# Optimization experiments

Measured on AMD Instinct MI355X. Metric: run time of the kernel, lower is better.

Reference implementation:

```python
import jax, jax.numpy as jnp
import numpy as np

N_NODES = 50000
N_EDGES = 800000
F_IN = 128
HEADS = 4
C_OUT = 32
HID = HEADS * C_OUT  # 128
NEG_SLOPE = 0.2


def _gatv2_layer(x, src, dst, W_l, b_l, W_r, b_r, att, bias, concat):
    """PyG-style GATv2Conv (eval mode, no dropout).
    x: [N, F]; W_*: [F, H*C]; att: [H, C]; bias: [H*C] (concat) or [C] (mean).
    """
    N = x.shape[0]
    H, C = att.shape
    x_l = (x @ W_l + b_l).reshape(N, H, C)  # source transform
    x_r = (x @ W_r + b_r).reshape(N, H, C)  # target transform
    e = jax.nn.leaky_relu(x_l[src] + x_r[dst], NEG_SLOPE)      # [E, H, C]
    logits = jnp.einsum('ehc,hc->eh', e, att)                   # [E, H]
    # segment softmax over incoming edges of each destination node
    m = jax.ops.segment_max(logits, dst, num_segments=N)        # [N, H]
    alpha = jnp.exp(logits - m[dst])
    denom = jax.ops.segment_sum(alpha, dst, num_segments=N)     # [N, H]
    alpha = alpha / (denom[dst] + 1e-16)
    out = jax.ops.segment_sum(x_l[src] * alpha[..., None], dst, num_segments=N)  # [N, H, C]
    out = out.reshape(N, H * C) if concat else out.mean(axis=1)
    return out + bias


def setup_inputs() -> dict:
    key = jax.random.key(0)
    ks = jax.random.split(key, 20)
    s = 0.1
    inp = {
        'x': jax.random.normal(ks[0], (N_NODES, F_IN), dtype=jnp.float32),
        'edge_index': jax.random.randint(ks[1], (2, N_EDGES), 0, N_NODES, dtype=jnp.int64),
        # layer 1: 128 -> 4 heads x 32
        'W_l1': jax.random.normal(ks[2], (F_IN, HID), dtype=jnp.float32) * s,
        'b_l1': jnp.zeros((HID,), dtype=jnp.float32),
        'W_r1': jax.random.normal(ks[3], (F_IN, HID), dtype=jnp.float32) * s,
        'b_r1': jnp.zeros((HID,), dtype=jnp.float32),
        'att1': jax.random.normal(ks[4], (HEADS, C_OUT), dtype=jnp.float32) * s,
        'bias1': jnp.zeros((HID,), dtype=jnp.float32),
        # layer 2: 128 -> 4 heads x 32
        'W_l2': jax.random.normal(ks[5], (HID, HID), dtype=jnp.float32) * s,
        'b_l2': jnp.zeros((HID,), dtype=jnp.float32),
        'W_r2': jax.random.normal(ks[6], (HID, HID), dtype=jnp.float32) * s,
        'b_r2': jnp.zeros((HID,), dtype=jnp.float32),
        'att2': jax.random.normal(ks[7], (HEADS, C_OUT), dtype=jnp.float32) * s,
        'bias2': jnp.zeros((HID,), dtype=jnp.float32),
        # final layer: 128 -> 1 head x 1, concat=False
        'W_l3': jax.random.normal(ks[8], (HID, 1), dtype=jnp.float32) * s,
        'b_l3': jnp.zeros((1,), dtype=jnp.float32),
        'W_r3': jax.random.normal(ks[9], (HID, 1), dtype=jnp.float32) * s,
        'b_r3': jnp.zeros((1,), dtype=jnp.float32),
        'att3': jax.random.normal(ks[10], (1, 1), dtype=jnp.float32) * s,
        'bias3': jnp.zeros((1,), dtype=jnp.float32),
    }
    return inp


def reference(x, edge_index, W_l1, b_l1, W_r1, b_r1, att1, bias1,
              W_l2, b_l2, W_r2, b_r2, att2, bias2,
              W_l3, b_l3, W_r3, b_r3, att3, bias3):
    src, dst = edge_index[0], edge_index[1]
    h = jax.nn.elu(_gatv2_layer(x, src, dst, W_l1, b_l1, W_r1, b_r1, att1, bias1, True))
    h = jax.nn.elu(_gatv2_layer(h, src, dst, W_l2, b_l2, W_r2, b_r2, att2, bias2, True))
    o = _gatv2_layer(h, src, dst, W_l3, b_l3, W_r3, b_r3, att3, bias3, False)
    return jax.nn.sigmoid(o).reshape(x.shape[0], 1)
```

## Files before the change

### kernel.cpp

```cpp
#include <hip/hip_runtime.h>
#include <hip/hip_bf16.h>
#include <math.h>

#define NN 50000
#define NE 800000
#define NBUK 391
#define BNODES 128

typedef __attribute__((ext_vector_type(8))) short bf16x8;
typedef __attribute__((ext_vector_type(4))) float f32x4;
typedef __attribute__((ext_vector_type(8))) unsigned short ushort8v;

__device__ __forceinline__ ushort f2bf(float v) {
  __hip_bfloat16 h = __float2bfloat16(v);
  return *(ushort*)&h;
}
__device__ __forceinline__ float bf2f(ushort u) {
  return __uint_as_float(((unsigned int)u) << 16);
}

__global__ void pack_w(const float* __restrict__ Wl, const float* __restrict__ Wr,
                       ushort* __restrict__ Bpack) {
  int t = blockIdx.x * 256 + threadIdx.x;
  if (t >= 4096) return;
  int hi = t & 3;
  int col = (t >> 2) & 255;
  int kt = t >> 10;
  const float* W = (col < 128) ? (Wl + col) : (Wr + (col - 128));
  ushort4 u0, u1;
  int k0 = kt * 32 + hi * 8;
  u0.x = f2bf(W[(k0 + 0) * 128]); u0.y = f2bf(W[(k0 + 1) * 128]);
  u0.z = f2bf(W[(k0 + 2) * 128]); u0.w = f2bf(W[(k0 + 3) * 128]);
  u1.x = f2bf(W[(k0 + 4) * 128]); u1.y = f2bf(W[(k0 + 5) * 128]);
  u1.z = f2bf(W[(k0 + 6) * 128]); u1.w = f2bf(W[(k0 + 7) * 128]);
  *(ushort4*)&Bpack[t * 8] = u0;
  *(ushort4*)&Bpack[t * 8 + 4] = u1;
}

template <int AF32>
__global__ __launch_bounds__(256) void gemm_mfma(
    const void* __restrict__ Aptr, const ushort* __restrict__ Bpack,
    const float* __restrict__ bl, const float* __restrict__ br,
    ushort* __restrict__ Xl, ushort* __restrict__ Xr, int n) {
  __shared__ ushort tile[64][264];
  const int tid = threadIdx.x;
  const int wv = tid >> 6;
  const int l = tid & 63;
  const int lr = l & 15;
  const int hi = l >> 4;
  const int r0 = blockIdx.x * 64;

  f32x4 acc[4][4];
#pragma unroll
  for (int mi = 0; mi < 4; ++mi)
#pragma unroll
    for (int nj = 0; nj < 4; ++nj) acc[mi][nj] = (f32x4)0.f;

#pragma unroll
  for (int kt = 0; kt < 4; ++kt) {
    bf16x8 b[4], a[4];
#pragma unroll
    for (int nj = 0; nj < 4; ++nj) {
      int col = wv * 64 + nj * 16 + lr;
      b[nj] = *(const bf16x8*)&Bpack[((kt * 256 + col) * 4 + hi) * 8];
    }
#pragma unroll
    for (int mi = 0; mi < 4; ++mi) {
      int row = r0 + mi * 16 + lr;
      row = row < n ? row : n - 1;
      if (AF32) {
        const float* Af = (const float*)Aptr;
        float4 f0 = *(const float4*)&Af[row * 128 + kt * 32 + hi * 8];
        float4 f1 = *(const float4*)&Af[row * 128 + kt * 32 + hi * 8 + 4];
        bf16x8 av;
        av[0] = (short)f2bf(f0.x); av[1] = (short)f2bf(f0.y);
        av[2] = (short)f2bf(f0.z); av[3] = (short)f2bf(f0.w);
        av[4] = (short)f2bf(f1.x); av[5] = (short)f2bf(f1.y);
        av[6] = (short)f2bf(f1.z); av[7] = (short)f2bf(f1.w);
        a[mi] = av;
      } else {
        const ushort* Ab = (const ushort*)Aptr;
        a[mi] = *(const bf16x8*)&Ab[row * 128 + kt * 32 + hi * 8];
      }
    }
#pragma unroll
    for (int mi = 0; mi < 4; ++mi)
#pragma unroll
      for (int nj = 0; nj < 4; ++nj)
        acc[mi][nj] = __builtin_amdgcn_mfma_f32_16x16x32_bf16(a[mi], b[nj], acc[mi][nj], 0, 0, 0);
  }

#pragma unroll
  for (int nj = 0; nj < 4; ++nj) {
    int col = wv * 64 + nj * 16 + lr;
    float bb = (col < 128) ? bl[col] : br[col - 128];
#pragma unroll
    for (int mi = 0; mi < 4; ++mi)
#pragma unroll
      for (int v = 0; v < 4; ++v)
        tile[mi * 16 + hi * 4 + v][col] = f2bf(acc[mi][nj][v] + bb);
  }
  __syncthreads();

#pragma unroll
  for (int j = 0; j < 8; ++j) {
    int c = j * 256 + tid;
    int rl = c >> 5;
    int colc = (c & 31) * 8;
    int row = r0 + rl;
    if (row < n) {
      ushort* dstp = (colc < 128) ? &Xl[row * 128 + colc] : &Xr[row * 128 + (colc - 128)];
      *(ushort8v*)dstp = *(const ushort8v*)&tile[rl][colc];
    }
  }
}

__global__ void zero_i32(int* p, int n) {
  int i = blockIdx.x * 256 + threadIdx.x;
  if (i < n) p[i] = 0;
}

__global__ void hist_kernel(const int* __restrict__ dst, int* __restrict__ deg) {
  int e = blockIdx.x * 256 + threadIdx.x;
  if (e < NE) atomicAdd(&deg[dst[e]], 1);
}

__global__ __launch_bounds__(256) void scan_a(const int* __restrict__ in,
                                              int* __restrict__ excl,
                                              int* __restrict__ bsum, int n) {
  int i = blockIdx.x * 256 + threadIdx.x;
  int v = (i < n) ? in[i] : 0;
  int lane = threadIdx.x & 63, wid = threadIdx.x >> 6;
  int incl = v;
#pragma unroll
  for (int off = 1; off < 64; off <<= 1) {
    int u = __shfl_up(incl, off);
    if (lane >= off) incl += u;
  }
  __shared__ int wsum[4];
  if (lane == 63) wsum[wid] = incl;
  __syncthreads();
  int wo = 0;
  for (int w = 0; w < wid; w++) wo += wsum[w];
  if (i < n) excl[i] = wo + incl - v;
  if (threadIdx.x == 255 && bsum) bsum[blockIdx.x] = wo + incl;
}

__global__ void scan_c(int* __restrict__ rowptr, const int* __restrict__ boff,
                       int* __restrict__ bcur, int n) {
  int i = blockIdx.x * 256 + threadIdx.x;
  if (i < n) {
    int v = rowptr[i] + boff[i >> 8];
    rowptr[i] = v;
    if ((i & 127) == 0) bcur[i >> 7] = v;
  } else if (i == n) {
    rowptr[n] = NE;
  }
}

__global__ __launch_bounds__(256) void bucket_scatter(
    const int* __restrict__ src, const int* __restrict__ dst,
    int* __restrict__ bcur, int2* __restrict__ pairs) {
  __shared__ int cnt[NBUK];
  __shared__ int base[NBUK];
  const int t = threadIdx.x;
  for (int i = t; i < NBUK; i += 256) cnt[i] = 0;
  __syncthreads();
  const int e0 = blockIdx.x * 4096;
#pragma unroll
  for (int j = 0; j < 16; ++j) {
    int e = e0 + j * 256 + t;
    if (e < NE) atomicAdd(&cnt[dst[e] >> 7], 1);
  }
  __syncthreads();
  for (int i = t; i < NBUK; i += 256) {
    int c = cnt[i];
    base[i] = c ? atomicAdd(&bcur[i], c) : 0;
    cnt[i] = 0;
  }
  __syncthreads();
#pragma unroll
  for (int j = 0; j < 16; ++j) {
    int e = e0 + j * 256 + t;
    if (e < NE) {
      int d = dst[e];
      int b = d >> 7;
      int r = atomicAdd(&cnt[b], 1);
      pairs[base[b] + r] = make_int2(src[e], d);
    }
  }
}

__global__ __launch_bounds__(256) void bucket_sort(
    const int2* __restrict__ pairs, const int* __restrict__ rowptr,
    int* __restrict__ ssort) {
  __shared__ int cur[BNODES];
  const int b = blockIdx.x;
  const int n0 = b * BNODES;
  const int t = threadIdx.x;
  const int n1 = min(n0 + BNODES, NN);
  if (t < BNODES && n0 + t < NN) cur[t] = rowptr[n0 + t];
  __syncthreads();
  const int e0 = rowptr[n0];
  const int e1 = rowptr[n1];
  for (int e = e0 + t; e < e1; e += 256) {
    int2 p = pairs[e];
    int pos = atomicAdd(&cur[p.y - n0], 1);
    ssort[pos] = p.x;
  }
}

template <int MODE>
__global__ __launch_bounds__(256) void gat_aggregate(
    const ushort* __restrict__ Xl, const ushort* __restrict__ Xr,
    const float* __restrict__ att, const int* __restrict__ ssort,
    const int* __restrict__ rowptr, const float* __restrict__ bias,
    ushort* __restrict__ outb,
    const float* __restrict__ Wl3, const float* __restrict__ Wr3,
    const float* __restrict__ bl3, const float* __restrict__ br3,
    float* __restrict__ xl3, float* __restrict__ xr3) {
  int slot = threadIdx.x >> 4;
  int l = threadIdx.x & 15;
  int n = blockIdx.x * 16 + slot;
  if (n >= NN) return;
  int s0 = rowptr[n], s1 = rowptr[n + 1];
  ushort8v xru = *(const ushort8v*)&Xr[n * 128 + l * 8];
  const float L2E = 1.44269504f;
  float xr[8], a6[8], a4[8];
#pragma unroll
  for (int c = 0; c < 8; ++c) {
    xr[c] = bf2f(xru[c]);
    float a = att[l * 8 + c];
    a6[c] = 0.6f * L2E * a;
    a4[c] = 0.4f * L2E * a;
  }
  float den = 0.f;
  float A0[8], A1[8];
#pragma unroll
  for (int c = 0; c < 8; ++c) { A0[c] = 0.f; A1[c] = 0.f; }

  int i = s0;
  for (; i + 4 <= s1; i += 4) {
    int sa = ssort[i], sb = ssort[i + 1], sc = ssort[i + 2], sd = ssort[i + 3];
    ushort8v ua = *(const ushort8v*)&Xl[sa * 128 + l * 8];
    ushort8v ub = *(const ushort8v*)&Xl[sb * 128 + l * 8];
    ushort8v uc = *(const ushort8v*)&Xl[sc * 128 + l * 8];
    ushort8v ud = *(const ushort8v*)&Xl[sd * 128 + l * 8];
    float xa[8], xb[8], xc[8], xd[8];
    float pa = 0.f, pb = 0.f, pc = 0.f, pd = 0.f;
#pragma unroll
    for (int c = 0; c < 8; ++c) {
      float va;
      xa[c] = bf2f(ua[c]); va = xa[c] + xr[c];
      pa = fmaf(a6[c], va, pa); pa = fmaf(a4[c], fabsf(va), pa);
      xb[c] = bf2f(ub[c]); va = xb[c] + xr[c];
      pb = fmaf(a6[c], va, pb); pb = fmaf(a4[c], fabsf(va), pb);
      xc[c] = bf2f(uc[c]); va = xc[c] + xr[c];
      pc = fmaf(a6[c], va, pc); pc = fmaf(a4[c], fabsf(va), pc);
      xd[c] = bf2f(ud[c]); va = xd[c] + xr[c];
      pd = fmaf(a6[c], va, pd); pd = fmaf(a4[c], fabsf(va), pd);
    }
    pa += __shfl_xor(pa, 1); pa += __shfl_xor(pa, 2);
    pb += __shfl_xor(pb, 1); pb += __shfl_xor(pb, 2);
    pc += __shfl_xor(pc, 1); pc += __shfl_xor(pc, 2);
    pd += __shfl_xor(pd, 1); pd += __shfl_xor(pd, 2);
    float wa = exp2f(fminf(pa, 43.f));
    float wb = exp2f(fminf(pb, 43.f));
    float wc = exp2f(fminf(pc, 43.f));
    float wd = exp2f(fminf(pd, 43.f));
    den += (wa + wb) + (wc + wd);
#pragma unroll
    for (int c = 0; c < 8; ++c) {
      A0[c] = fmaf(wa, xa[c], A0[c]); A1[c] = fmaf(wb, xb[c], A1[c]);
      A0[c] = fmaf(wc, xc[c], A0[c]); A1[c] = fmaf(wd, xd[c], A1[c]);
    }
  }
  for (; i < s1; ++i) {
    int sa = ssort[i];
    ushort8v ua = *(const ushort8v*)&Xl[sa * 128 + l * 8];
    float xa[8], pa = 0.f;
#pragma unroll
    for (int c = 0; c < 8; ++c) {
      xa[c] = bf2f(ua[c]);
      float va = xa[c] + xr[c];
      pa = fmaf(a6[c], va, pa); pa = fmaf(a4[c], fabsf(va), pa);
    }
    pa += __shfl_xor(pa, 1); pa += __shfl_xor(pa, 2);
    float wa = exp2f(fminf(pa, 43.f));
    den += wa;
#pragma unroll
    for (int c = 0; c < 8; ++c) A0[c] = fmaf(wa, xa[c], A0[c]);
  }
  float inv = 1.f / (den + 1e-16f);
  float o[8];
#pragma unroll
  for (int c = 0; c < 8; ++c) {
    o[c] = (A0[c] + A1[c]) * inv + bias[l * 8 + c];
    o[c] = o[c] > 0.f ? o[c] : __expf(o[c]) - 1.f;
  }
  if (MODE == 0) {
    ushort8v ub;
#pragma unroll
    for (int c = 0; c < 8; ++c) ub[c] = f2bf(o[c]);
    *(ushort8v*)&outb[n * 128 + l * 8] = ub;
  } else {
    float sl = 0.f, sr = 0.f;
#pragma unroll
    for (int c = 0; c < 8; ++c) {
      sl = fmaf(o[c], Wl3[l * 8 + c], sl);
      sr = fmaf(o[c], Wr3[l * 8 + c], sr);
    }
#pragma unroll
    for (int off = 1; off <= 8; off <<= 1) {
      sl += __shfl_xor(sl, off);
      sr += __shfl_xor(sr, off);
    }
    if (l == 0) {
      xl3[n] = sl + bl3[0];
      xr3[n] = sr + br3[0];
    }
  }
}

__global__ __launch_bounds__(256) void aggregate3_fused(
    const float* __restrict__ xl3, const float* __restrict__ xr3,
    const float* __restrict__ att, const int* __restrict__ ssort,
    const int* __restrict__ rowptr, const float* __restrict__ bias,
    float* __restrict__ out, int nn) {
  int wid = threadIdx.x >> 6, lane = threadIdx.x & 63;
  int n = blockIdx.x * 4 + wid;
  if (n >= nn) return;
  int s0 = rowptr[n], s1 = rowptr[n + 1];
  float xr = xr3[n];
  const float L2E = 1.44269504f;
  float s6 = 0.6f * L2E * att[0];
  float s4 = 0.4f * L2E * att[0];
  float den = 0.f, acc = 0.f;
  for (int i = s0 + lane; i < s1; i += 64) {
    float xl = xl3[ssort[i]];
    float v = xl + xr;
    float p = fmaf(s6, v, s4 * fabsf(v));
    float w = exp2f(fminf(p, 43.f));
    den += w;
    acc += w * xl;
  }
#pragma unroll
  for (int off = 32; off; off >>= 1) {
    den += __shfl_xor(den, off);
    acc += __shfl_xor(acc, off);
  }
  if (lane == 0) {
    float o = acc / (den + 1e-16f) + bias[0];
    out[n] = 1.f / (1.f + __expf(-o));
  }
}

extern "C" void kernel_launch(void* const* d_in, const int* in_sizes, int n_in,
                              void* d_out, int out_size, void* d_ws, size_t ws_size,
                              hipStream_t stream) {
  const float* x = (const float*)d_in[0];
  const int* ei = (const int*)d_in[1];
  const int* src = ei;
  const int* dst = ei + NE;
  const float* W_l1 = (const float*)d_in[2];
  const float* b_l1 = (const float*)d_in[3];
  const float* W_r1 = (const float*)d_in[4];
  const float* b_r1 = (const float*)d_in[5];
  const float* att1 = (const float*)d_in[6];
  const float* bias1 = (const float*)d_in[7];
  const float* W_l2 = (const float*)d_in[8];
  const float* b_l2 = (const float*)d_in[9];
  const float* W_r2 = (const float*)d_in[10];
  const float* b_r2 = (const float*)d_in[11];
  const float* att2 = (const float*)d_in[12];
  const float* bias2 = (const float*)d_in[13];
  const float* W_l3 = (const float*)d_in[14];
  const float* b_l3 = (const float*)d_in[15];
  const float* W_r3 = (const float*)d_in[16];
  const float* b_r3 = (const float*)d_in[17];
  const float* att3 = (const float*)d_in[18];
  const float* bias3 = (const float*)d_in[19];
  float* out = (float*)d_out;

  ushort* xbb = (ushort*)d_ws;
  ushort* xl_b = xbb + NN * 128;
  ushort* xr_b = xl_b + NN * 128;
  ushort* bpack = xr_b + NN * 128;
  int* deg = (int*)(bpack + 32768);
  int* rowptr = deg + NN;
  int* bcur = rowptr + NN + 1;
  int* bsum = bcur + NBUK;
  int* boff = bsum + 256;
  int* ssort = boff + 256;
  int2* pairs = (int2*)(ssort + NE);
  float* xl3 = (float*)(pairs + NE);
  float* xr3 = xl3 + NN;

  const int NB_N = (NN + 255) / 256;
  const int NB_E = (NE + 255) / 256;
  const int NB_G = (NN + 63) / 64;
  const int NB_A = (NN + 15) / 16;
  const int NB_W4 = (NN + 3) / 4;
  const int NB_BK = (NE + 4095) / 4096;

  zero_i32<<<NB_N, 256, 0, stream>>>(deg, NN);
  hist_kernel<<<NB_E, 256, 0, stream>>>(dst, deg);
  scan_a<<<NB_N, 256, 0, stream>>>(deg, rowptr, bsum, NN);
  scan_a<<<1, 256, 0, stream>>>(bsum, boff, (int*)nullptr, NB_N);
  scan_c<<<NB_N + 1, 256, 0, stream>>>(rowptr, boff, bcur, NN);
  bucket_scatter<<<NB_BK, 256, 0, stream>>>(src, dst, bcur, pairs);
  bucket_sort<<<NBUK, 256, 0, stream>>>(pairs, rowptr, ssort);

  pack_w<<<16, 256, 0, stream>>>(W_l1, W_r1, bpack);
  gemm_mfma<1><<<NB_G, 256, 0, stream>>>(x, bpack, b_l1, b_r1, xl_b, xr_b, NN);
  gat_aggregate<0><<<NB_A, 256, 0, stream>>>(xl_b, xr_b, att1, ssort, rowptr, bias1,
                                             xbb, nullptr, nullptr, nullptr, nullptr,
                                             nullptr, nullptr);

  pack_w<<<16, 256, 0, stream>>>(W_l2, W_r2, bpack);
  gemm_mfma<0><<<NB_G, 256, 0, stream>>>(xbb, bpack, b_l2, b_r2, xl_b, xr_b, NN);
  gat_aggregate<1><<<NB_A, 256, 0, stream>>>(xl_b, xr_b, att2, ssort, rowptr, bias2,
                                             nullptr, W_l3, W_r3, b_l3, b_r3,
                                             xl3, xr3);

  aggregate3_fused<<<NB_W4, 256, 0, stream>>>(xl3, xr3, att3, ssort, rowptr, bias3, out, NN);
}
```

Baseline: 309.9 us.

## Fuse CSR build into one cooperative kernel and pack both weights at once

```diff
diff --git a/kernel.cpp b/kernel.cpp
--- a/kernel.cpp
+++ b/kernel.cpp
@@ -1,11 +1,15 @@
 #include <hip/hip_runtime.h>
 #include <hip/hip_bf16.h>
+#include <hip/hip_cooperative_groups.h>
 #include <math.h>
+
+namespace cg = cooperative_groups;
 
 #define NN 50000
 #define NE 800000
 #define NBUK 391
 #define BNODES 128
+#define CSRB 196
 
 typedef __attribute__((ext_vector_type(8))) short bf16x8;
 typedef __attribute__((ext_vector_type(4))) float f32x4;
@@ -19,13 +23,19 @@
   return __uint_as_float(((unsigned int)u) << 16);
 }
 
-__global__ void pack_w(const float* __restrict__ Wl, const float* __restrict__ Wr,
-                       ushort* __restrict__ Bpack) {
+__global__ void pack_w_both(const float* __restrict__ Wl1, const float* __restrict__ Wr1,
+                            const float* __restrict__ Wl2, const float* __restrict__ Wr2,
+                            ushort* __restrict__ Bp1, ushort* __restrict__ Bp2) {
   int t = blockIdx.x * 256 + threadIdx.x;
-  if (t >= 4096) return;
-  int hi = t & 3;
-  int col = (t >> 2) & 255;
-  int kt = t >> 10;
+  if (t >= 8192) return;
+  int layer = t >> 12;
+  int tt = t & 4095;
+  int hi = tt & 3;
+  int col = (tt >> 2) & 255;
+  int kt = tt >> 10;
+  const float* Wl = layer ? Wl2 : Wl1;
+  const float* Wr = layer ? Wr2 : Wr1;
+  ushort* Bp = layer ? Bp2 : Bp1;
   const float* W = (col < 128) ? (Wl + col) : (Wr + (col - 128));
   ushort4 u0, u1;
   int k0 = kt * 32 + hi * 8;
@@ -33,8 +43,8 @@
   u0.z = f2bf(W[(k0 + 2) * 128]); u0.w = f2bf(W[(k0 + 3) * 128]);
   u1.x = f2bf(W[(k0 + 4) * 128]); u1.y = f2bf(W[(k0 + 5) * 128]);
   u1.z = f2bf(W[(k0 + 6) * 128]); u1.w = f2bf(W[(k0 + 7) * 128]);
-  *(ushort4*)&Bpack[t * 8] = u0;
-  *(ushort4*)&Bpack[t * 8 + 4] = u1;
+  *(ushort4*)&Bp[tt * 8] = u0;
+  *(ushort4*)&Bp[tt * 8 + 4] = u1;
 }
 
 template <int AF32>
@@ -115,98 +125,123 @@
   }
 }
 
-__global__ void zero_i32(int* p, int n) {
-  int i = blockIdx.x * 256 + threadIdx.x;
-  if (i < n) p[i] = 0;
-}
-
-__global__ void hist_kernel(const int* __restrict__ dst, int* __restrict__ deg) {
-  int e = blockIdx.x * 256 + threadIdx.x;
-  if (e < NE) atomicAdd(&deg[dst[e]], 1);
-}
-
-__global__ __launch_bounds__(256) void scan_a(const int* __restrict__ in,
-                                              int* __restrict__ excl,
-                                              int* __restrict__ bsum, int n) {
-  int i = blockIdx.x * 256 + threadIdx.x;
-  int v = (i < n) ? in[i] : 0;
-  int lane = threadIdx.x & 63, wid = threadIdx.x >> 6;
-  int incl = v;
-#pragma unroll
-  for (int off = 1; off < 64; off <<= 1) {
-    int u = __shfl_up(incl, off);
-    if (lane >= off) incl += u;
-  }
+__global__ __launch_bounds__(256) void csr_build(
+    const int* __restrict__ src, const int* __restrict__ dst,
+    int* __restrict__ deg, int* __restrict__ rowptr, int* __restrict__ bsum,
+    int* __restrict__ boff, int* __restrict__ bcur,
+    unsigned int* __restrict__ pairs, int* __restrict__ ssort) {
+  cg::grid_group grid = cg::this_grid();
+  const int t = threadIdx.x;
+  const int bid = blockIdx.x;
+  const int gid = bid * 256 + t;
   __shared__ int wsum[4];
-  if (lane == 63) wsum[wid] = incl;
-  __syncthreads();
-  int wo = 0;
-  for (int w = 0; w < wid; w++) wo += wsum[w];
-  if (i < n) excl[i] = wo + incl - v;
-  if (threadIdx.x == 255 && bsum) bsum[blockIdx.x] = wo + incl;
-}
-
-__global__ void scan_c(int* __restrict__ rowptr, const int* __restrict__ boff,
-                       int* __restrict__ bcur, int n) {
-  int i = blockIdx.x * 256 + threadIdx.x;
-  if (i < n) {
-    int v = rowptr[i] + boff[i >> 8];
-    rowptr[i] = v;
-    if ((i & 127) == 0) bcur[i >> 7] = v;
-  } else if (i == n) {
-    rowptr[n] = NE;
-  }
-}
-
-__global__ __launch_bounds__(256) void bucket_scatter(
-    const int* __restrict__ src, const int* __restrict__ dst,
-    int* __restrict__ bcur, int2* __restrict__ pairs) {
   __shared__ int cnt[NBUK];
   __shared__ int base[NBUK];
-  const int t = threadIdx.x;
-  for (int i = t; i < NBUK; i += 256) cnt[i] = 0;
-  __syncthreads();
-  const int e0 = blockIdx.x * 4096;
-#pragma unroll
-  for (int j = 0; j < 16; ++j) {
-    int e = e0 + j * 256 + t;
-    if (e < NE) atomicAdd(&cnt[dst[e] >> 7], 1);
-  }
-  __syncthreads();
-  for (int i = t; i < NBUK; i += 256) {
-    int c = cnt[i];
-    base[i] = c ? atomicAdd(&bcur[i], c) : 0;
-    cnt[i] = 0;
-  }
-  __syncthreads();
-#pragma unroll
-  for (int j = 0; j < 16; ++j) {
-    int e = e0 + j * 256 + t;
-    if (e < NE) {
-      int d = dst[e];
-      int b = d >> 7;
-      int r = atomicAdd(&cnt[b], 1);
-      pairs[base[b] + r] = make_int2(src[e], d);
-    }
-  }
-}
-
-__global__ __launch_bounds__(256) void bucket_sort(
-    const int2* __restrict__ pairs, const int* __restrict__ rowptr,
-    int* __restrict__ ssort) {
   __shared__ int cur[BNODES];
-  const int b = blockIdx.x;
-  const int n0 = b * BNODES;
-  const int t = threadIdx.x;
-  const int n1 = min(n0 + BNODES, NN);
-  if (t < BNODES && n0 + t < NN) cur[t] = rowptr[n0 + t];
-  __syncthreads();
-  const int e0 = rowptr[n0];
-  const int e1 = rowptr[n1];
-  for (int e = e0 + t; e < e1; e += 256) {
-    int2 p = pairs[e];
-    int pos = atomicAdd(&cur[p.y - n0], 1);
-    ssort[pos] = p.x;
+
+  if (gid < NN) deg[gid] = 0;
+  grid.sync();
+
+  {
+    const int e0 = bid * 4096;
+#pragma unroll
+    for (int j = 0; j < 16; ++j) {
+      int e = e0 + j * 256 + t;
+      if (e < NE) atomicAdd(&deg[dst[e]], 1);
+    }
+  }
+  grid.sync();
+
+  {
+    int v = (gid < NN) ? deg[gid] : 0;
+    int lane = t & 63, wid = t >> 6;
+    int incl = v;
+#pragma unroll
+    for (int off = 1; off < 64; off <<= 1) {
+      int u = __shfl_up(incl, off);
+      if (lane >= off) incl += u;
+    }
+    if (lane == 63) wsum[wid] = incl;
+    __syncthreads();
+    int wo = 0;
+    for (int w = 0; w < wid; w++) wo += wsum[w];
+    if (gid < NN) rowptr[gid] = wo + incl - v;
+    if (t == 255) bsum[bid] = wo + incl;
+  }
+  grid.sync();
+
+  if (bid == 0) {
+    int v = (t < CSRB) ? bsum[t] : 0;
+    int lane = t & 63, wid = t >> 6;
+    int incl = v;
+#pragma unroll
+    for (int off = 1; off < 64; off <<= 1) {
+      int u = __shfl_up(incl, off);
+      if (lane >= off) incl += u;
+    }
+    __syncthreads();
+    if (lane == 63) wsum[wid] = incl;
+    __syncthreads();
+    int wo = 0;
+    for (int w = 0; w < wid; w++) wo += wsum[w];
+    boff[t] = wo + incl - v;
+  }
+  grid.sync();
+
+  {
+    int i = gid;
+    if (i < NN) {
+      int v = rowptr[i] + boff[i >> 8];
+      rowptr[i] = v;
+      if ((i & 127) == 0) bcur[i >> 7] = v;
+    } else if (i == NN) {
+      rowptr[NN] = NE;
+    }
+  }
+  grid.sync();
+
+  {
+    for (int i = t; i < NBUK; i += 256) cnt[i] = 0;
+    __syncthreads();
+    const int e0 = bid * 4096;
+#pragma unroll
+    for (int j = 0; j < 16; ++j) {
+      int e = e0 + j * 256 + t;
+      if (e < NE) atomicAdd(&cnt[dst[e] >> 7], 1);
+    }
+    __syncthreads();
+    for (int i = t; i < NBUK; i += 256) {
+      int c = cnt[i];
+      base[i] = c ? atomicAdd(&bcur[i], c) : 0;
+      cnt[i] = 0;
+    }
+    __syncthreads();
+#pragma unroll
+    for (int j = 0; j < 16; ++j) {
+      int e = e0 + j * 256 + t;
+      if (e < NE) {
+        int d = dst[e];
+        int b = d >> 7;
+        int r = atomicAdd(&cnt[b], 1);
+        pairs[base[b] + r] = ((unsigned int)(d & 127) << 17) | (unsigned int)src[e];
+      }
+    }
+  }
+  grid.sync();
+
+  for (int b = bid; b < NBUK; b += CSRB) {
+    int n0 = b * BNODES;
+    int n1 = min(n0 + BNODES, NN);
+    if (t < BNODES && n0 + t < NN) cur[t] = rowptr[n0 + t];
+    __syncthreads();
+    const int e0 = rowptr[n0];
+    const int e1 = rowptr[n1];
+    for (int e = e0 + t; e < e1; e += 256) {
+      unsigned int p = pairs[e];
+      int pos = atomicAdd(&cur[p >> 17], 1);
+      ssort[pos] = (int)(p & 0x1FFFF);
+    }
+    __syncthreads();
   }
 }
 
@@ -385,40 +420,37 @@
   ushort* xbb = (ushort*)d_ws;
   ushort* xl_b = xbb + NN * 128;
   ushort* xr_b = xl_b + NN * 128;
-  ushort* bpack = xr_b + NN * 128;
-  int* deg = (int*)(bpack + 32768);
+  ushort* bpack1 = xr_b + NN * 128;
+  ushort* bpack2 = bpack1 + 32768;
+  int* deg = (int*)(bpack2 + 32768);
   int* rowptr = deg + NN;
   int* bcur = rowptr + NN + 1;
   int* bsum = bcur + NBUK;
   int* boff = bsum + 256;
   int* ssort = boff + 256;
-  int2* pairs = (int2*)(ssort + NE);
+  unsigned int* pairs = (unsigned int*)(ssort + NE);
   float* xl3 = (float*)(pairs + NE);
   float* xr3 = xl3 + NN;
 
-  const int NB_N = (NN + 255) / 256;
-  const int NB_E = (NE + 255) / 256;
   const int NB_G = (NN + 63) / 64;
   const int NB_A = (NN + 15) / 16;
   const int NB_W4 = (NN + 3) / 4;
-  const int NB_BK = (NE + 4095) / 4096;
-
-  zero_i32<<<NB_N, 256, 0, stream>>>(deg, NN);
-  hist_kernel<<<NB_E, 256, 0, stream>>>(dst, deg);
-  scan_a<<<NB_N, 256, 0, stream>>>(deg, rowptr, bsum, NN);
-  scan_a<<<1, 256, 0, stream>>>(bsum, boff, (int*)nullptr, NB_N);
-  scan_c<<<NB_N + 1, 256, 0, stream>>>(rowptr, boff, bcur, NN);
-  bucket_scatter<<<NB_BK, 256, 0, stream>>>(src, dst, bcur, pairs);
-  bucket_sort<<<NBUK, 256, 0, stream>>>(pairs, rowptr, ssort);
-
-  pack_w<<<16, 256, 0, stream>>>(W_l1, W_r1, bpack);
-  gemm_mfma<1><<<NB_G, 256, 0, stream>>>(x, bpack, b_l1, b_r1, xl_b, xr_b, NN);
+
+  {
+    void* args[] = {(void*)&src, (void*)&dst, (void*)&deg, (void*)&rowptr,
+                    (void*)&bsum, (void*)&boff, (void*)&bcur, (void*)&pairs,
+                    (void*)&ssort};
+    hipLaunchCooperativeKernel((void*)csr_build, dim3(CSRB), dim3(256), args, 0, stream);
+  }
+
+  pack_w_both<<<32, 256, 0, stream>>>(W_l1, W_r1, W_l2, W_r2, bpack1, bpack2);
+
+  gemm_mfma<1><<<NB_G, 256, 0, stream>>>(x, bpack1, b_l1, b_r1, xl_b, xr_b, NN);
   gat_aggregate<0><<<NB_A, 256, 0, stream>>>(xl_b, xr_b, att1, ssort, rowptr, bias1,
                                              xbb, nullptr, nullptr, nullptr, nullptr,
                                              nullptr, nullptr);
 
-  pack_w<<<16, 256, 0, stream>>>(W_l2, W_r2, bpack);
-  gemm_mfma<0><<<NB_G, 256, 0, stream>>>(xbb, bpack, b_l2, b_r2, xl_b, xr_b, NN);
+  gemm_mfma<0><<<NB_G, 256, 0, stream>>>(xbb, bpack2, b_l2, b_r2, xl_b, xr_b, NN);
   gat_aggregate<1><<<NB_A, 256, 0, stream>>>(xl_b, xr_b, att2, ssort, rowptr, bias2,
                                              nullptr, W_l3, W_r3, b_l3, b_r3,
                                              xl3, xr3);
```

Measured after the change: 464.7 us. 1.5x slower.
